# Optimization experiments

Measured on AMD Instinct MI355X. Metric: run time of the kernel, lower is better.

Reference implementation:

```python
import jax, jax.numpy as jnp
import numpy as np

K = 3          # kernel_size
S = 2          # stride
NEW = 2        # new_size = int(ratio * stride)
C = 32         # channels
BN_EPS = 1e-5


def _unfold(x, oh, ow):
    # torch.nn.Unfold(K, dilation=1, padding=(K-1)//2, stride=S) reshaped to
    # [B, C, K, K, oh, ow] (channel slowest, then kernel rows, kernel cols).
    p = (K - 1) // 2
    xp = jnp.pad(x, ((0, 0), (0, 0), (p, p), (p, p)))
    rows = []
    for i in range(K):
        cols = []
        for j in range(K):
            cols.append(xp[:, :, i:i + S * (oh - 1) + 1:S, j:j + S * (ow - 1) + 1:S])
        rows.append(jnp.stack(cols, axis=2))          # [B,C,K,oh,ow]
    return jnp.stack(rows, axis=2)                    # [B,C,K,K,oh,ow]


def reference(x, conv_w, bn_gamma, bn_beta, bn_mean, bn_var):
    B, _, W, H = x.shape
    oh = -(-W // S)
    ow = -(-H // S)
    patches = _unfold(x, oh, ow)                      # [B,C,K,K,oh,ow]

    # three max reductions over different unfolded axes
    x1 = patches.max(axis=1).reshape(B, K * K, oh, ow)    # over channels
    x2 = patches.max(axis=2).reshape(B, C * K, oh, ow)    # over kernel rows
    x3 = patches.max(axis=3).reshape(B, C * K, oh, ow)    # over kernel cols
    feat = jnp.concatenate([x1, x2, x3], axis=1)          # [B, K*K+2*C*K, oh, ow]

    # ConvModule: 1x1 conv (no bias, since BN) -> BN (eval stats) -> ReLU
    y = jnp.einsum('bihw,oi->bohw', feat, conv_w)
    inv = (bn_gamma / jnp.sqrt(bn_var + BN_EPS))[None, :, None, None]
    y = (y - bn_mean[None, :, None, None]) * inv + bn_beta[None, :, None, None]
    y = jax.nn.relu(y)

    # dynamic kernel: [B, C, K*K, NEW, NEW, oh, ow]
    w = y.reshape(B, C, K * K, NEW, NEW, oh, ow)
    px = patches.reshape(B, C, K * K, 1, 1, oh, ow)
    out = jnp.mean(px * w, axis=2)                    # [B,C,NEW,NEW,oh,ow]
    out = out.transpose(0, 1, 4, 2, 5, 3)             # [B,C,oh,NEW,ow,NEW]
    out = out.reshape(B, C, oh * NEW, ow * NEW)
    return out[:, :, :W, :H]


def setup_inputs() -> dict:
    key = jax.random.key(0)
    k1, k2 = jax.random.split(key)
    B, W, H = 8, 128, 128
    in_ch = K * C * 2 + K * K                         # 201
    out_ch = C * NEW * NEW * K * K                    # 1152
    x = jax.random.normal(k1, (B, C, W, H), dtype=jnp.float32)
    conv_w = jax.random.normal(k2, (out_ch, in_ch), dtype=jnp.float32) * 0.02
    return {
        'x': x,
        'conv_w': conv_w,
        'bn_gamma': jnp.ones((out_ch,), jnp.float32),
        'bn_beta': jnp.zeros((out_ch,), jnp.float32),
        'bn_mean': jnp.zeros((out_ch,), jnp.float32),
        'bn_var': jnp.ones((out_ch,), jnp.float32),
    }
```

## Files before the change

kernel.cpp:

```cpp
#include <hip/hip_runtime.h>
#include <math.h>

typedef __bf16 v8bf __attribute__((ext_vector_type(8)));
typedef float  v4f  __attribute__((ext_vector_type(4)));

constexpr int Bsz  = 8;
constexpr int Cch  = 32;
constexpr int WIMG = 128;
constexpr int OH   = 64;
constexpr int OW   = 64;
constexpr int INCH = 201;
constexpr int KP   = 224;
constexpr int NK   = 7;
constexpr int OUTCH = 1152;
constexpr int MTOT = Bsz * OH * OW;
constexpr float BN_EPS = 1e-5f;

constexpr size_t WT_BYTES = (size_t)NK * OUTCH * 32 * 2;
constexpr size_t BIAS_OFF = WT_BYTES;
constexpr size_t FEAT_OFF = BIAS_OFF + OUTCH * 4;

typedef const void __attribute__((address_space(1)))* gas_ptr;
typedef void __attribute__((address_space(3)))* las_ptr;
__device__ __forceinline__ void load16_lds(const void* g, void* l) {
    __builtin_amdgcn_global_load_lds((gas_ptr)(uintptr_t)g, (las_ptr)(uintptr_t)l, 16, 0, 0);
}

constexpr int SXS = 132;
constexpr int FEAT_BLOCKS = Bsz * OH;
constexpr int NPREP = OUTCH * KP + OUTCH;
constexpr int PREP_BLOCKS = (NPREP + 255) / 256;

__global__ __launch_bounds__(256)
void prep_feat_kernel(const float* __restrict__ x,
                      const float* __restrict__ conv_w,
                      const float* __restrict__ gamma,
                      const float* __restrict__ beta,
                      const float* __restrict__ mean,
                      const float* __restrict__ var,
                      __bf16* __restrict__ Wt,
                      float* __restrict__ biasp,
                      __bf16* __restrict__ feat) {
    __shared__ __align__(16) float sx[Cch * 3 * SXS];
    __shared__ __align__(16) float cmax[3 * SXS];
    __shared__ __align__(16) __bf16 sfeat[NK * OW * 32];

    const int t = threadIdx.x;

    if (blockIdx.x >= FEAT_BLOCKS) {
        int idx = ((int)blockIdx.x - FEAT_BLOCKS) * 256 + t;
        const int nW = OUTCH * KP;
        if (idx < nW) {
            int o = idx / KP;
            int f = idx - o * KP;
            float inv = gamma[o] * rsqrtf(var[o] + BN_EPS);
            float v = (f < INCH) ? conv_w[o * INCH + f] * inv : 0.0f;
            Wt[((size_t)(f >> 5) * OUTCH + o) * 32 + (f & 31)] = (__bf16)v;
        } else if (idx < nW + OUTCH) {
            int o = idx - nW;
            float inv = gamma[o] * rsqrtf(var[o] + BN_EPS);
            biasp[o] = beta[o] - mean[o] * inv;
        }
        return;
    }

    const int b  = blockIdx.x >> 6;
    const int ho = blockIdx.x & 63;

    for (int idx = t; idx < Cch * 3 * 32; idx += 256) {
        int c   = idx / 96;
        int rem = idx - c * 96;
        int i   = rem >> 5;
        int q   = rem & 31;
        int r   = 2 * ho - 1 + i;
        float4 v = make_float4(0.f, 0.f, 0.f, 0.f);
        if (r >= 0 && r < WIMG)
            v = *(const float4*)(x + (((size_t)(b * Cch + c) * WIMG) + r) * WIMG + q * 4);
        float* dst = sx + (c * 3 + i) * SXS + q * 4 + 1;
        dst[0] = v.x; dst[1] = v.y; dst[2] = v.z; dst[3] = v.w;
    }
    if (t < 96) {
        float* row = sx + t * SXS;
        row[0] = 0.0f; row[129] = 0.0f; row[130] = 0.0f; row[131] = 0.0f;
    }
    __syncthreads();

    if (t < 99) {
        int i = t / 33, cg = t - i * 33;
        const float4* base = (const float4*)sx + i * (SXS / 4) + cg;
        float4 m = base[0];
        #pragma unroll 4
        for (int c = 1; c < Cch; ++c) {
            float4 v = base[(size_t)c * (3 * SXS / 4)];
            m.x = fmaxf(m.x, v.x); m.y = fmaxf(m.y, v.y);
            m.z = fmaxf(m.z, v.z); m.w = fmaxf(m.w, v.w);
        }
        ((float4*)cmax)[i * (SXS / 4) + cg] = m;
    }
    __syncthreads();

    for (int idx = t; idx < 9 * 64; idx += 256) {
        int f = idx >> 6, wo = idx & 63;
        int i = f / 3, j = f - 3 * i;
        sfeat[wo * 32 + f] = (__bf16)cmax[i * SXS + 2 * wo + j];
    }
    {
        const int wp = t & 31, g = t >> 5;
        const int wo0 = 2 * wp;
        #pragma unroll
        for (int cl = 0; cl < 4; ++cl) {
            int c = g * 4 + cl;
            float v[3][5];
            #pragma unroll
            for (int i = 0; i < 3; ++i) {
                const float* row = sx + (c * 3 + i) * SXS + 4 * wp;
                float4 q = *(const float4*)row;
                v[i][0] = q.x; v[i][1] = q.y; v[i][2] = q.z; v[i][3] = q.w;
                v[i][4] = row[4];
            }
            #pragma unroll
            for (int i = 0; i < 3; ++i) {
                int f = 105 + c * 3 + i;
                float a0 = fmaxf(fmaxf(v[i][0], v[i][1]), v[i][2]);
                float a1 = fmaxf(fmaxf(v[i][2], v[i][3]), v[i][4]);
                sfeat[(f >> 5) * 2048 + wo0 * 32 + (f & 31)]       = (__bf16)a0;
                sfeat[(f >> 5) * 2048 + (wo0 + 1) * 32 + (f & 31)] = (__bf16)a1;
            }
            #pragma unroll
            for (int j = 0; j < 3; ++j) {
                int f = 9 + c * 3 + j;
                float a0 = fmaxf(fmaxf(v[0][j], v[1][j]), v[2][j]);
                float a1 = fmaxf(fmaxf(v[0][j + 2], v[1][j + 2]), v[2][j + 2]);
                sfeat[(f >> 5) * 2048 + wo0 * 32 + (f & 31)]       = (__bf16)a0;
                sfeat[(f >> 5) * 2048 + (wo0 + 1) * 32 + (f & 31)] = (__bf16)a1;
            }
        }
    }
    for (int idx = t; idx < 64 * 23; idx += 256) {
        int wo = idx / 23, fo = idx - wo * 23;
        int f = 201 + fo;
        sfeat[6 * 2048 + wo * 32 + (f & 31)] = (__bf16)0.0f;
    }
    __syncthreads();

    const size_t spat0 = (size_t)(b * OH + ho) * OW;
    #pragma unroll
    for (int kc = 0; kc < NK; ++kc) {
        float4 vv = ((const float4*)sfeat)[kc * 256 + t];
        ((float4*)((char*)feat + ((size_t)kc * MTOT + spat0) * 64))[t] = vv;
    }
}

constexpr int YS  = 148;
constexpr int REG = 16 * YS;
__global__ __launch_bounds__(256, 2)
void gemm_kernel(const __bf16* __restrict__ feat,
                 const __bf16* __restrict__ Wt,
                 const float* __restrict__ biasp,
                 const float* __restrict__ x,
                 float* __restrict__ out) {
    __shared__ __align__(16) unsigned char lds[37888];

    const int t    = threadIdx.x;
    const int nb   = (int)blockIdx.x >> 8;
    const int mb   = (int)blockIdx.x & 255;
    const int M0   = mb * 128;
    const int N0   = nb * 144;
    const int wave = t >> 6, lane = t & 63, quad = lane >> 4, l16 = lane & 15;

    auto issue = [&](int ks, int buf) {
        const char* Ag = (const char*)feat + ((size_t)ks * MTOT + M0) * 64;
        char* Ab = (char*)lds + buf * 8192;
        #pragma unroll
        for (int i = 0; i < 2; ++i) {
            int off = (wave * 2 + i) * 1024 + lane * 16;
            load16_lds(Ag + off, Ab + off);
        }
        const char* Bg = (const char*)Wt + ((size_t)ks * OUTCH + N0) * 64;
        char* Bb = (char*)lds + 16384 + buf * 9216;
        #pragma unroll
        for (int i = 0; i < 2; ++i) {
            int off = (wave * 2 + i) * 1024 + lane * 16;
            load16_lds(Bg + off, Bb + off);
        }
        if (wave == 0) {
            int off2 = 8192 + lane * 16;
            load16_lds(Bg + off2, Bb + off2);
        }
    };

    v4f acc[2][9];
    #pragma unroll
    for (int mt = 0; mt < 2; ++mt)
        #pragma unroll
        for (int nt = 0; nt < 9; ++nt)
            acc[mt][nt] = (v4f){0.f, 0.f, 0.f, 0.f};

    issue(0, 0);
    __syncthreads();

    for (int ks = 0; ks < NK; ++ks) {
        const int cur = ks & 1;
        if (ks + 1 < NK) issue(ks + 1, cur ^ 1);

        const char* Ab = (const char*)lds + cur * 8192;
        const char* Bb = (const char*)lds + 16384 + cur * 9216;
        v8bf af[2];
        #pragma unroll
        for (int mt = 0; mt < 2; ++mt)
            af[mt] = *(const v8bf*)(Ab + (wave * 32 + mt * 16 + l16) * 64 + quad * 16);
        #pragma unroll
        for (int nt = 0; nt < 9; ++nt) {
            v8bf bf = *(const v8bf*)(Bb + (nt * 16 + l16) * 64 + quad * 16);
            #pragma unroll
            for (int mt = 0; mt < 2; ++mt)
                acc[mt][nt] = __builtin_amdgcn_mfma_f32_16x16x32_bf16(
                    af[mt], bf, acc[mt][nt], 0, 0, 0);
        }
        __syncthreads();
    }

    float bia[9];
    #pragma unroll
    for (int nt = 0; nt < 9; ++nt) bia[nt] = biasp[N0 + nt * 16 + l16];

    float* yw = (float*)lds + wave * REG;
    const int cl  = lane >> 4;
    const int wl  = lane & 15;
    const int cg  = nb * 4 + cl;
    const float s9 = 1.0f / 9.0f;

    #pragma unroll
    for (int p = 0; p < 2; ++p) {
        #pragma unroll
        for (int nt = 0; nt < 9; ++nt)
            #pragma unroll
            for (int r = 0; r < 4; ++r)
                yw[(quad * 4 + r) * YS + nt * 16 + l16] =
                    fmaxf(acc[p][nt][r] + bia[nt], 0.0f);

        const int mg  = M0 + wave * 32 + p * 16 + wl;
        const int bb  = mg >> 12;
        const int hob = (mg >> 6) & 63;
        const int wo  = mg & 63;
        const float* xc = x + (size_t)(bb * Cch + cg) * WIMG * WIMG;

        float pt[9];
        #pragma unroll
        for (int qi = 0; qi < 3; ++qi) {
            int r = 2 * hob - 1 + qi;
            #pragma unroll
            for (int qj = 0; qj < 3; ++qj) {
                int col = 2 * wo - 1 + qj;
                float v = 0.0f;
                if (r >= 0 && r < WIMG && col >= 0 && col < WIMG)
                    v = xc[r * WIMG + col];
                pt[qi * 3 + qj] = v;
            }
        }
        const float4* yrow = (const float4*)(yw + wl * YS + cl * 36);
        float o00 = 0.f, o01 = 0.f, o10 = 0.f, o11 = 0.f;
        #pragma unroll
        for (int q = 0; q < 9; ++q) {
            float4 yv = yrow[q];
            float pq = pt[q];
            o00 = fmaf(pq, yv.x, o00);
            o01 = fmaf(pq, yv.y, o01);
            o10 = fmaf(pq, yv.z, o10);
            o11 = fmaf(pq, yv.w, o11);
        }
        size_t obase = (((size_t)(bb * Cch + cg) * WIMG) + 2 * hob) * WIMG + 2 * wo;
        *(float2*)(out + obase)        = make_float2(o00 * s9, o01 * s9);
        *(float2*)(out + obase + WIMG) = make_float2(o10 * s9, o11 * s9);
    }
}

extern "C" void kernel_launch(void* const* d_in, const int* in_sizes, int n_in,
                              void* d_out, int out_size, void* d_ws, size_t ws_size,
                              hipStream_t stream) {
    const float* x      = (const float*)d_in[0];
    const float* conv_w = (const float*)d_in[1];
    const float* gamma  = (const float*)d_in[2];
    const float* beta   = (const float*)d_in[3];
    const float* mean   = (const float*)d_in[4];
    const float* var    = (const float*)d_in[5];
    float* out = (float*)d_out;

    __bf16* Wt    = (__bf16*)d_ws;
    float*  biasp = (float*)((char*)d_ws + BIAS_OFF);
    __bf16* feat  = (__bf16*)((char*)d_ws + FEAT_OFF);

    prep_feat_kernel<<<FEAT_BLOCKS + PREP_BLOCKS, 256, 0, stream>>>(
        x, conv_w, gamma, beta, mean, var, Wt, biasp, feat);
    gemm_kernel<<<(OUTCH / 144) * (MTOT / 128), 256, 0, stream>>>(feat, Wt, biasp, x, out);
}
```

Before: 118.4 us.

## Restructure GEMM to 6-wave 2x3 tiling with whole-B LDS preload and register-direct A

```diff
diff --git a/kernel.cpp b/kernel.cpp
--- a/kernel.cpp
+++ b/kernel.cpp
@@ -151,15 +151,14 @@
     }
 }
 
-constexpr int YS  = 148;
-constexpr int REG = 16 * YS;
-__global__ __launch_bounds__(256, 2)
+constexpr int YS = 148;
+__global__ __launch_bounds__(384, 3)
 void gemm_kernel(const __bf16* __restrict__ feat,
                  const __bf16* __restrict__ Wt,
                  const float* __restrict__ biasp,
                  const float* __restrict__ x,
                  float* __restrict__ out) {
-    __shared__ __align__(16) unsigned char lds[37888];
+    __shared__ __align__(16) unsigned char lds[128 * YS * 4];
 
     const int t    = threadIdx.x;
     const int nb   = (int)blockIdx.x >> 8;
@@ -167,82 +166,97 @@
     const int M0   = mb * 128;
     const int N0   = nb * 144;
     const int wave = t >> 6, lane = t & 63, quad = lane >> 4, l16 = lane & 15;
-
-    auto issue = [&](int ks, int buf) {
-        const char* Ag = (const char*)feat + ((size_t)ks * MTOT + M0) * 64;
-        char* Ab = (char*)lds + buf * 8192;
-        #pragma unroll
-        for (int i = 0; i < 2; ++i) {
-            int off = (wave * 2 + i) * 1024 + lane * 16;
-            load16_lds(Ag + off, Ab + off);
-        }
-        const char* Bg = (const char*)Wt + ((size_t)ks * OUTCH + N0) * 64;
-        char* Bb = (char*)lds + 16384 + buf * 9216;
-        #pragma unroll
-        for (int i = 0; i < 2; ++i) {
-            int off = (wave * 2 + i) * 1024 + lane * 16;
-            load16_lds(Bg + off, Bb + off);
-        }
-        if (wave == 0) {
-            int off2 = 8192 + lane * 16;
-            load16_lds(Bg + off2, Bb + off2);
-        }
+    const int wm   = wave / 3;
+    const int wn   = wave - 3 * wm;
+
+    {
+        const char* Bg = (const char*)Wt + (size_t)N0 * 64;
+        #pragma unroll
+        for (int i = wave; i < 63; i += 6) {
+            int ks = i / 9, sub = i - ks * 9;
+            load16_lds(Bg + (size_t)ks * (OUTCH * 64) + sub * 1024 + lane * 16,
+                       (char*)lds + i * 1024 + lane * 16);
+        }
+    }
+
+    const char* Ag = (const char*)feat;
+    const int arow0 = M0 + wm * 64 + l16;
+    auto loadA = [&](v8bf (&buf)[4], int ks) {
+        #pragma unroll
+        for (int mt = 0; mt < 4; ++mt)
+            buf[mt] = *(const v8bf*)(Ag +
+                ((size_t)ks * MTOT + arow0 + mt * 16) * 64 + quad * 16);
     };
-
-    v4f acc[2][9];
-    #pragma unroll
-    for (int mt = 0; mt < 2; ++mt)
-        #pragma unroll
-        for (int nt = 0; nt < 9; ++nt)
+    const char* Bb = (const char*)lds;
+    auto loadB = [&](v8bf (&buf)[3], int ks) {
+        #pragma unroll
+        for (int nt = 0; nt < 3; ++nt)
+            buf[nt] = *(const v8bf*)(Bb + ks * 9216 +
+                (wn * 48 + nt * 16 + l16) * 64 + quad * 16);
+    };
+
+    v4f acc[4][3];
+    #pragma unroll
+    for (int mt = 0; mt < 4; ++mt)
+        #pragma unroll
+        for (int nt = 0; nt < 3; ++nt)
             acc[mt][nt] = (v4f){0.f, 0.f, 0.f, 0.f};
 
-    issue(0, 0);
-    __syncthreads();
-
-    for (int ks = 0; ks < NK; ++ks) {
-        const int cur = ks & 1;
-        if (ks + 1 < NK) issue(ks + 1, cur ^ 1);
-
-        const char* Ab = (const char*)lds + cur * 8192;
-        const char* Bb = (const char*)lds + 16384 + cur * 9216;
-        v8bf af[2];
-        #pragma unroll
-        for (int mt = 0; mt < 2; ++mt)
-            af[mt] = *(const v8bf*)(Ab + (wave * 32 + mt * 16 + l16) * 64 + quad * 16);
-        #pragma unroll
-        for (int nt = 0; nt < 9; ++nt) {
-            v8bf bf = *(const v8bf*)(Bb + (nt * 16 + l16) * 64 + quad * 16);
-            #pragma unroll
-            for (int mt = 0; mt < 2; ++mt)
+    v8bf afA[4], afB[4], bfA[3], bfB[3];
+    loadA(afA, 0);
+    loadA(afB, 1);
+    __syncthreads();
+    loadB(bfA, 0);
+
+    auto mfma12 = [&](v8bf (&af)[4], v8bf (&bf)[3]) {
+        #pragma unroll
+        for (int nt = 0; nt < 3; ++nt)
+            #pragma unroll
+            for (int mt = 0; mt < 4; ++mt)
                 acc[mt][nt] = __builtin_amdgcn_mfma_f32_16x16x32_bf16(
-                    af[mt], bf, acc[mt][nt], 0, 0, 0);
-        }
-        __syncthreads();
-    }
-
-    float bia[9];
-    #pragma unroll
-    for (int nt = 0; nt < 9; ++nt) bia[nt] = biasp[N0 + nt * 16 + l16];
-
-    float* yw = (float*)lds + wave * REG;
-    const int cl  = lane >> 4;
-    const int wl  = lane & 15;
-    const int cg  = nb * 4 + cl;
+                    af[mt], bf[nt], acc[mt][nt], 0, 0, 0);
+    };
+
+    #pragma unroll 1
+    for (int ks = 0; ks < 6; ks += 2) {
+        loadB(bfB, ks + 1);
+        mfma12(afA, bfA);
+        loadA(afA, ks + 2);
+        loadB(bfA, ks + 2);
+        mfma12(afB, bfB);
+        if (ks + 3 < NK) loadA(afB, ks + 3);
+    }
+    mfma12(afA, bfA);
+
+    float bia[3];
+    #pragma unroll
+    for (int nt = 0; nt < 3; ++nt)
+        bia[nt] = biasp[N0 + wn * 48 + nt * 16 + l16];
+
+    __syncthreads();
+    float* y = (float*)lds;
+    #pragma unroll
+    for (int mt = 0; mt < 4; ++mt)
+        #pragma unroll
+        for (int nt = 0; nt < 3; ++nt)
+            #pragma unroll
+            for (int r = 0; r < 4; ++r)
+                y[(wm * 64 + mt * 16 + quad * 4 + r) * YS + wn * 48 + nt * 16 + l16] =
+                    fmaxf(acc[mt][nt][r] + bia[nt], 0.0f);
+    __syncthreads();
+
     const float s9 = 1.0f / 9.0f;
-
-    #pragma unroll
-    for (int p = 0; p < 2; ++p) {
-        #pragma unroll
-        for (int nt = 0; nt < 9; ++nt)
-            #pragma unroll
-            for (int r = 0; r < 4; ++r)
-                yw[(quad * 4 + r) * YS + nt * 16 + l16] =
-                    fmaxf(acc[p][nt][r] + bia[nt], 0.0f);
-
-        const int mg  = M0 + wave * 32 + p * 16 + wl;
-        const int bb  = mg >> 12;
-        const int hob = (mg >> 6) & 63;
-        const int wo  = mg & 63;
+    #pragma unroll
+    for (int pass = 0; pass < 2; ++pass) {
+        int it = t + pass * 384;
+        if (pass == 1 && t >= 128) break;
+        const int chl  = it >> 7;
+        const int mloc = it & 127;
+        const int mg   = M0 + mloc;
+        const int bb   = mg >> 12;
+        const int hob  = (mg >> 6) & 63;
+        const int wo   = mg & 63;
+        const int cg   = nb * 4 + chl;
         const float* xc = x + (size_t)(bb * Cch + cg) * WIMG * WIMG;
 
         float pt[9];
@@ -258,7 +272,7 @@
                 pt[qi * 3 + qj] = v;
             }
         }
-        const float4* yrow = (const float4*)(yw + wl * YS + cl * 36);
+        const float4* yrow = (const float4*)(y + mloc * YS + chl * 36);
         float o00 = 0.f, o01 = 0.f, o10 = 0.f, o11 = 0.f;
         #pragma unroll
         for (int q = 0; q < 9; ++q) {
@@ -292,5 +306,5 @@
 
     prep_feat_kernel<<<FEAT_BLOCKS + PREP_BLOCKS, 256, 0, stream>>>(
         x, conv_w, gamma, beta, mean, var, Wt, biasp, feat);
-    gemm_kernel<<<(OUTCH / 144) * (MTOT / 128), 256, 0, stream>>>(feat, Wt, biasp, x, out);
+    gemm_kernel<<<(OUTCH / 144) * (MTOT / 128), 384, 0, stream>>>(feat, Wt, biasp, x, out);
 }
```

Measured after the change: 140.2 us. 1.18x slower.
